# Kernel optimization log

Measured on AMD Instinct MI355X. Metric: run time of the kernel, lower is better.

## Reference

```python
import jax, jax.numpy as jnp
import numpy as np

EPS = 1e-6
LAMBDA_INIT = 0.8

def rmsnorm(x, g):
    return x * jax.lax.rsqrt(jnp.mean(x * x, axis=-1, keepdims=True) + EPS) * g

def diff_attention(q_in, kv_in, Wq, Wk, Wv, Wo, lq1, lk1, lq2, lk2, causal):
    # q_in: [B,T,D], kv_in: [B,S,D]; Wq/Wk: [D, H*2*hs], Wv: [D, H*hs], Wo: [H*hs, D]
    B, T, _ = q_in.shape
    S = kv_in.shape[1]
    H, hs = lq1.shape
    q = (q_in @ Wq).reshape(B, T, H, 2, hs)
    k = (kv_in @ Wk).reshape(B, S, H, 2, hs)
    v = (kv_in @ Wv).reshape(B, S, H, hs)
    q1, q2 = q[..., 0, :], q[..., 1, :]
    k1, k2 = k[..., 0, :], k[..., 1, :]
    scale = 1.0 / np.sqrt(hs).astype(np.float32)
    a1 = jnp.einsum('bthd,bshd->bhts', q1, k1) * scale  # [B,H,T,S]
    a2 = jnp.einsum('bthd,bshd->bhts', q2, k2) * scale
    if causal:
        mask = jnp.tril(jnp.ones((T, S), dtype=bool))
        neg = jnp.asarray(-1e9, a1.dtype)
        a1 = jnp.where(mask, a1, neg)
        a2 = jnp.where(mask, a2, neg)
    s1 = jax.nn.softmax(a1, axis=-1)
    s2 = jax.nn.softmax(a2, axis=-1)
    lam = jnp.exp(jnp.sum(lq1 * lk1, -1)) - jnp.exp(jnp.sum(lq2 * lk2, -1)) + LAMBDA_INIT  # [H]
    attn = s1 - lam[None, :, None, None] * s2
    o = jnp.einsum('bhts,bshd->bthd', attn, v)  # [B,T,H,hs]
    # per-head RMSNorm (no affine) scaled by (1 - lambda_init), per Diff Transformer
    o = o * jax.lax.rsqrt(jnp.mean(o * o, -1, keepdims=True) + EPS) * (1.0 - LAMBDA_INIT)
    return o.reshape(B, T, H * hs) @ Wo

def swiglu(x, W1, W2, W3):
    return (jax.nn.silu(x @ W1) * (x @ W2)) @ W3

def setup_inputs():
    B, T, D, H, hs = 4, 1024, 1024, 16, 64
    Dff = 4 * D
    ks = jax.random.split(jax.random.key(0), 24)
    w = lambda i, shape, s=0.02: (jax.random.normal(ks[i], shape, jnp.float32) * s)
    return {
        'x': jax.random.normal(ks[0], (B, T, D), jnp.float32),
        'encoder_output': jax.random.normal(ks[1], (B, T, D), jnp.float32),
        'Wq_s': w(2, (D, H * 2 * hs)), 'Wk_s': w(3, (D, H * 2 * hs)),
        'Wv_s': w(4, (D, H * hs)), 'Wo_s': w(5, (H * hs, D)),
        'lq1_s': w(6, (H, hs), 0.1), 'lk1_s': w(7, (H, hs), 0.1),
        'lq2_s': w(8, (H, hs), 0.1), 'lk2_s': w(9, (H, hs), 0.1),
        'Wq_c': w(10, (D, H * 2 * hs)), 'Wk_c': w(11, (D, H * 2 * hs)),
        'Wv_c': w(12, (D, H * hs)), 'Wo_c': w(13, (H * hs, D)),
        'lq1_c': w(14, (H, hs), 0.1), 'lk1_c': w(15, (H, hs), 0.1),
        'lq2_c': w(16, (H, hs), 0.1), 'lk2_c': w(17, (H, hs), 0.1),
        'g_rms': jnp.ones((D,), jnp.float32),
        'W1': w(18, (D, Dff)), 'W2': w(19, (D, Dff)), 'W3': w(20, (Dff, D)),
    }

def reference(x, encoder_output, Wq_s, Wk_s, Wv_s, Wo_s, lq1_s, lk1_s, lq2_s, lk2_s,
              Wq_c, Wk_c, Wv_c, Wo_c, lq1_c, lk1_c, lq2_c, lk2_c,
              g_rms, W1, W2, W3):
    # dropout prob 0.0 -> identity (eval/reference mode)
    h = rmsnorm(x, g_rms)
    h = diff_attention(h, h, Wq_s, Wk_s, Wv_s, Wo_s, lq1_s, lk1_s, lq2_s, lk2_s, causal=True) + h
    h = diff_attention(h, encoder_output, Wq_c, Wk_c, Wv_c, Wo_c, lq1_c, lk1_c, lq2_c, lk2_c, causal=False)
    h = h + h  # faithful to source: out = dropout(out) + out after cross-attention
    h = swiglu(rmsnorm(h, g_rms), W1, W2, W3) + h
    return h
```

## Files before the change

### kernel.cpp

```cpp
#include <hip/hip_runtime.h>

typedef __attribute__((ext_vector_type(8))) short s16x8;
typedef __attribute__((ext_vector_type(4))) float f32x4;
typedef unsigned short u16;

__device__ __forceinline__ float bu2f(u16 u) {
    union { unsigned int i; float f; } x; x.i = ((unsigned int)u) << 16; return x.f;
}
__device__ __forceinline__ u16 f2bu(float f) {
    union { float f; unsigned int i; } x; x.f = f;
    unsigned int r = x.i + 0x7fffu + ((x.i >> 16) & 1u);
    return (u16)(r >> 16);
}

__device__ __forceinline__ void gld_lds16(const void* g, void* l) {
    __builtin_amdgcn_global_load_lds(
        (const __attribute__((address_space(1))) unsigned int*)g,
        (__attribute__((address_space(3))) unsigned int*)l, 16, 0, 0);
}
#define WAIT_VM0()   asm volatile("s_waitcnt vmcnt(0)" ::: "memory")
#define WAIT_LGKM0() asm volatile("s_waitcnt lgkmcnt(0)" ::: "memory")
#define MEMBAR()     asm volatile("" ::: "memory")

__global__ __launch_bounds__(256)
void transpose_k(const float* __restrict__ src, u16* __restrict__ dst, int R, int C) {
    __shared__ u16 t[32][33];
    int bx = blockIdx.x * 32, by = blockIdx.y * 32;
    int x = bx + threadIdx.x;
#pragma unroll
    for (int k = 0; k < 4; ++k)
        t[threadIdx.y + k * 8][threadIdx.x] = f2bu(src[(size_t)(by + threadIdx.y + k * 8) * C + x]);
    __syncthreads();
    int x2 = by + threadIdx.x;
#pragma unroll
    for (int k = 0; k < 4; ++k)
        dst[(size_t)(bx + threadIdx.y + k * 8) * R + x2] = t[threadIdx.x][threadIdx.y + k * 8];
}

__global__ __launch_bounds__(256)
void convert_k(const float* __restrict__ a, u16* __restrict__ o, int n4) {
    int i = blockIdx.x * 256 + threadIdx.x;
    if (i >= n4) return;
    float4 v = ((const float4*)a)[i];
    ushort4 u;
    u.x = f2bu(v.x); u.y = f2bu(v.y); u.z = f2bu(v.z); u.w = f2bu(v.w);
    ((ushort4*)o)[i] = u;
}

__global__ __launch_bounds__(256)
void rmsnorm_k(const float* __restrict__ x, const float* __restrict__ g, u16* __restrict__ y) {
    const int row = blockIdx.x, tid = threadIdx.x;
    float4 v = ((const float4*)(x + (size_t)row * 1024))[tid];
    float ss = v.x * v.x + v.y * v.y + v.z * v.z + v.w * v.w;
#pragma unroll
    for (int off = 32; off; off >>= 1) ss += __shfl_xor(ss, off, 64);
    __shared__ float red[4];
    if ((tid & 63) == 0) red[tid >> 6] = ss;
    __syncthreads();
    float tot = red[0] + red[1] + red[2] + red[3];
    float sc = rsqrtf(tot * (1.f / 1024.f) + 1e-6f);
    float4 gv = ((const float4*)g)[tid];
    ushort4 o;
    o.x = f2bu(v.x * sc * gv.x);
    o.y = f2bu(v.y * sc * gv.y);
    o.z = f2bu(v.z * sc * gv.z);
    o.w = f2bu(v.w * sc * gv.w);
    ((ushort4*)(y + (size_t)row * 1024))[tid] = o;
}

__global__ __launch_bounds__(256)
void silumul_k(const u16* __restrict__ a, const u16* __restrict__ b, u16* __restrict__ o, int n4) {
    int i = blockIdx.x * 256 + threadIdx.x;
    if (i >= n4) return;
    ushort4 ua = ((const ushort4*)a)[i], ub = ((const ushort4*)b)[i];
    ushort4 uo;
    {
        float v = bu2f(ua.x); uo.x = f2bu(v / (1.f + __expf(-v)) * bu2f(ub.x));
        v = bu2f(ua.y); uo.y = f2bu(v / (1.f + __expf(-v)) * bu2f(ub.y));
        v = bu2f(ua.z); uo.z = f2bu(v / (1.f + __expf(-v)) * bu2f(ub.z));
        v = bu2f(ua.w); uo.w = f2bu(v / (1.f + __expf(-v)) * bu2f(ub.w));
    }
    ((ushort4*)o)[i] = uo;
}

template <int TM>
__global__ __launch_bounds__(256, 2)
void gemm_bt(const u16* __restrict__ A, const u16* __restrict__ Bt, void* __restrict__ C,
             const void* __restrict__ res, int M, int N, int K, int mode) {
    constexpr int MI = TM / 32;
    __shared__ u16 sA[TM * 32];
    __shared__ u16 sB[128 * 32];
    const int tid = threadIdx.x;
    const int w = tid >> 6, lane = tid & 63, q4 = lane >> 4, l16 = lane & 15;
    const int m0 = blockIdx.y * TM, n0 = blockIdx.x * 128;
    const int wm = (w >> 1) * (TM / 2), wn = (w & 1) * 64;

    const f32x4 fzero = {0.f, 0.f, 0.f, 0.f};
    f32x4 acc[MI][4];
#pragma unroll
    for (int i = 0; i < MI; ++i)
#pragma unroll
        for (int j = 0; j < 4; ++j) acc[i][j] = fzero;

    const int r0 = tid >> 2, c0 = (tid & 3) * 8;

    for (int k0 = 0; k0 < K; k0 += 32) {
        gld_lds16(A + (size_t)(m0 + r0) * K + k0 + c0, &sA[tid * 8]);
        if (TM == 128)
            gld_lds16(A + (size_t)(m0 + 64 + r0) * K + k0 + c0, &sA[(256 + tid) * 8]);
        gld_lds16(Bt + (size_t)(n0 + r0) * K + k0 + c0, &sB[tid * 8]);
        gld_lds16(Bt + (size_t)(n0 + 64 + r0) * K + k0 + c0, &sB[(256 + tid) * 8]);
        WAIT_VM0();
        __syncthreads();
        s16x8 af[MI], bfr[4];
#pragma unroll
        for (int i = 0; i < MI; ++i) af[i] = *(const s16x8*)&sA[(wm + i * 16 + l16) * 32 + q4 * 8];
#pragma unroll
        for (int j = 0; j < 4; ++j) bfr[j] = *(const s16x8*)&sB[(wn + j * 16 + l16) * 32 + q4 * 8];
#pragma unroll
        for (int i = 0; i < MI; ++i)
#pragma unroll
            for (int j = 0; j < 4; ++j)
                acc[i][j] = __builtin_amdgcn_mfma_f32_16x16x32_bf16(af[i], bfr[j], acc[i][j], 0, 0, 0);
        __syncthreads();
    }

    const size_t QBSZ = (size_t)4096 * 2048;
    const size_t FSZ  = (size_t)4096 * 4096;
#pragma unroll
    for (int i = 0; i < MI; ++i)
#pragma unroll
        for (int j = 0; j < 4; ++j)
#pragma unroll
            for (int r = 0; r < 4; ++r) {
                int m = m0 + wm + i * 16 + q4 * 4 + r;
                int n = n0 + wn + j * 16 + l16;
                float v = acc[i][j][r];
                if (mode == 0) {
                    ((u16*)C)[(size_t)m * N + n] = f2bu(v);
                } else if (mode == 1) {
                    ((u16*)C)[(size_t)m * N + n] = f2bu(v + bu2f(((const u16*)res)[(size_t)m * N + n]));
                } else if (mode == 2) {
                    ((float*)C)[(size_t)m * N + n] = 2.f * v;
                } else if (mode == 4) {
                    ((float*)C)[(size_t)m * N + n] = v + ((const float*)res)[(size_t)m * N + n];
                } else if (mode == 5) {
                    if (n < 2048) ((u16*)C)[(size_t)m * 2048 + n] = f2bu(v);
                    else if (n < 4096) ((u16*)C)[QBSZ + (size_t)m * 2048 + (n - 2048)] = f2bu(v);
                    else {
                        int nn = n - 4096, hh = nn >> 6, d = nn & 63, b = m >> 10, s = m & 1023;
                        ((u16*)C)[2 * QBSZ + ((size_t)((b * 16 + hh) * 64 + d)) * 1024 + s] = f2bu(v);
                    }
                } else if (mode == 6) {
                    if (n < 2048) ((u16*)C)[(size_t)m * 2048 + n] = f2bu(v);
                    else {
                        int nn = n - 2048, hh = nn >> 6, d = nn & 63, b = m >> 10, s = m & 1023;
                        ((u16*)C)[QBSZ + ((size_t)((b * 16 + hh) * 64 + d)) * 1024 + s] = f2bu(v);
                    }
                } else {
                    if (n < 4096) ((u16*)C)[(size_t)m * 4096 + n] = f2bu(v);
                    else ((u16*)C)[FSZ + (size_t)m * 4096 + (n - 4096)] = f2bu(v);
                }
            }
}

template <bool CAUSAL>
__global__ __launch_bounds__(256, 2)
void diff_flash(const u16* __restrict__ Q, const u16* __restrict__ Kg, const u16* __restrict__ Vt,
                u16* __restrict__ O, const float* __restrict__ lq1, const float* __restrict__ lk1,
                const float* __restrict__ lq2, const float* __restrict__ lk2, int T, int S) {
    __shared__ u16 sK1[2][64 * 64];
    __shared__ u16 sK2[2][64 * 64];
    __shared__ u16 sV[2][64 * 64];
    __shared__ u16 sP[4][16 * 72];

    const int tid = threadIdx.x;
    const int w = tid >> 6, lane = tid & 63, q4 = lane >> 4, l16 = lane & 15;
    const int h = blockIdx.x, b = blockIdx.y, zt = blockIdx.z, t0 = zt * 64;
    const f32x4 fzero = {0.f, 0.f, 0.f, 0.f};

    float d1 = 0.f, d2 = 0.f;
    for (int d = 0; d < 64; ++d) {
        d1 += lq1[h * 64 + d] * lk1[h * 64 + d];
        d2 += lq2[h * 64 + d] * lk2[h * 64 + d];
    }
    const float lam = __expf(d1) - __expf(d2) + 0.8f;

    s16x8 qf[2][2];
    {
        const size_t qrow = (size_t)(b * T + t0 + w * 16 + l16) * 2048 + h * 128;
#pragma unroll
        for (int c = 0; c < 2; ++c)
#pragma unroll
            for (int kk = 0; kk < 2; ++kk)
                qf[c][kk] = *(const s16x8*)&Q[qrow + c * 64 + kk * 32 + q4 * 8];
    }

    f32x4 o1[4], o2[4];
    float ms1[4], ls1[4], ms2[4], ls2[4];
#pragma unroll
    for (int jn = 0; jn < 4; ++jn) { o1[jn] = fzero; o2[jn] = fzero; }
#pragma unroll
    for (int r = 0; r < 4; ++r) { ms1[r] = ms2[r] = -1e30f; ls1[r] = ls2[r] = 0.f; }

    const int ntiles = CAUSAL ? (zt + 1) : (S / 64);
    const int rk = tid >> 3, ck = (tid & 7) * 8;

    auto stage = [&](int buf, int s0) {
        const size_t kb = (size_t)(b * S + s0 + rk) * 2048 + h * 128 + ck;
        gld_lds16(&Kg[kb], &sK1[buf][tid * 8]);
        gld_lds16(&Kg[kb + (size_t)32 * 2048], &sK1[buf][(256 + tid) * 8]);
        gld_lds16(&Kg[kb + 64], &sK2[buf][tid * 8]);
        gld_lds16(&Kg[kb + (size_t)32 * 2048 + 64], &sK2[buf][(256 + tid) * 8]);
        const size_t vb = (size_t)((b * 16 + h) * 64 + rk) * 1024 + s0 + ck;
        gld_lds16(&Vt[vb], &sV[buf][tid * 8]);
        gld_lds16(&Vt[vb + (size_t)32 * 1024], &sV[buf][(256 + tid) * 8]);
    };

    stage(0, 0);
    for (int it = 0; it < ntiles; ++it) {
        WAIT_VM0();
        __syncthreads();
        if (it + 1 < ntiles) stage((it + 1) & 1, (it + 1) * 64);
        const int buf = it & 1, s0 = it * 64;
        const bool diag = CAUSAL && (it == ntiles - 1);

        auto comp_step = [&](const u16* sK, const u16* sVb, const s16x8* qfc,
                             float* m, float* l, f32x4* o) {
            f32x4 sc[4];
#pragma unroll
            for (int j = 0; j < 4; ++j) sc[j] = fzero;
#pragma unroll
            for (int j = 0; j < 4; ++j)
#pragma unroll
                for (int kk = 0; kk < 2; ++kk) {
                    s16x8 kf = *(const s16x8*)&sK[(j * 16 + l16) * 64 + kk * 32 + q4 * 8];
                    sc[j] = __builtin_amdgcn_mfma_f32_16x16x32_bf16(qfc[kk], kf, sc[j], 0, 0, 0);
                }
            float p[4][4];
#pragma unroll
            for (int j = 0; j < 4; ++j)
#pragma unroll
                for (int r = 0; r < 4; ++r) {
                    float v = sc[j][r] * 0.125f;
                    if (diag && (s0 + j * 16 + l16 > t0 + w * 16 + q4 * 4 + r)) v = -1e9f;
                    p[j][r] = v;
                }
            float mx[4];
#pragma unroll
            for (int r = 0; r < 4; ++r)
                mx[r] = fmaxf(fmaxf(p[0][r], p[1][r]), fmaxf(p[2][r], p[3][r]));
#pragma unroll
            for (int off = 8; off; off >>= 1)
#pragma unroll
                for (int r = 0; r < 4; ++r) mx[r] = fmaxf(mx[r], __shfl_xor(mx[r], off, 16));
            float alpha[4];
#pragma unroll
            for (int r = 0; r < 4; ++r) {
                float mn = fmaxf(m[r], mx[r]);
                alpha[r] = __expf(m[r] - mn);
                m[r] = mn;
            }
            float rs[4];
#pragma unroll
            for (int r = 0; r < 4; ++r) {
                float s0r = 0.f;
#pragma unroll
                for (int j = 0; j < 4; ++j) { p[j][r] = __expf(p[j][r] - m[r]); s0r += p[j][r]; }
                rs[r] = s0r;
            }
#pragma unroll
            for (int off = 8; off; off >>= 1)
#pragma unroll
                for (int r = 0; r < 4; ++r) rs[r] += __shfl_xor(rs[r], off, 16);
#pragma unroll
            for (int r = 0; r < 4; ++r) l[r] = l[r] * alpha[r] + rs[r];
#pragma unroll
            for (int jn = 0; jn < 4; ++jn)
#pragma unroll
                for (int r = 0; r < 4; ++r) o[jn][r] *= alpha[r];
#pragma unroll
            for (int j = 0; j < 4; ++j)
#pragma unroll
                for (int r = 0; r < 4; ++r)
                    sP[w][(q4 * 4 + r) * 72 + j * 16 + l16] = f2bu(p[j][r]);
            WAIT_LGKM0();
            s16x8 pa0 = *(const s16x8*)&sP[w][l16 * 72 + q4 * 8];
            s16x8 pa1 = *(const s16x8*)&sP[w][l16 * 72 + 32 + q4 * 8];
#pragma unroll
            for (int jn = 0; jn < 4; ++jn) {
                s16x8 vf0 = *(const s16x8*)&sVb[(jn * 16 + l16) * 64 + q4 * 8];
                o[jn] = __builtin_amdgcn_mfma_f32_16x16x32_bf16(pa0, vf0, o[jn], 0, 0, 0);
                s16x8 vf1 = *(const s16x8*)&sVb[(jn * 16 + l16) * 64 + 32 + q4 * 8];
                o[jn] = __builtin_amdgcn_mfma_f32_16x16x32_bf16(pa1, vf1, o[jn], 0, 0, 0);
            }
            MEMBAR();
        };
        comp_step(sK1[buf], sV[buf], qf[0], ms1, ls1, o1);
        comp_step(sK2[buf], sV[buf], qf[1], ms2, ls2, o2);
    }

    float inv1[4], inv2[4];
#pragma unroll
    for (int r = 0; r < 4; ++r) { inv1[r] = 1.f / ls1[r]; inv2[r] = lam / ls2[r]; }
    float val[4][4];
    float ss[4] = {0.f, 0.f, 0.f, 0.f};
#pragma unroll
    for (int jn = 0; jn < 4; ++jn)
#pragma unroll
        for (int r = 0; r < 4; ++r) {
            float v = o1[jn][r] * inv1[r] - o2[jn][r] * inv2[r];
            val[jn][r] = v;
            ss[r] += v * v;
        }
#pragma unroll
    for (int off = 8; off; off >>= 1)
#pragma unroll
        for (int r = 0; r < 4; ++r) ss[r] += __shfl_xor(ss[r], off, 16);
#pragma unroll
    for (int r = 0; r < 4; ++r) ss[r] = rsqrtf(ss[r] * (1.f / 64.f) + 1e-6f) * 0.2f;
#pragma unroll
    for (int jn = 0; jn < 4; ++jn)
#pragma unroll
        for (int r = 0; r < 4; ++r)
            O[(size_t)(b * T + t0 + w * 16 + q4 * 4 + r) * 1024 + h * 64 + jn * 16 + l16] =
                f2bu(val[jn][r] * ss[r]);
}

extern "C" void kernel_launch(void* const* d_in, const int* in_sizes, int n_in,
                              void* d_out, int out_size, void* d_ws, size_t ws_size,
                              hipStream_t stream) {
    (void)in_sizes; (void)n_in; (void)out_size; (void)ws_size;
    const float* x     = (const float*)d_in[0];
    const float* enc   = (const float*)d_in[1];
    const float* Wq_s  = (const float*)d_in[2];
    const float* Wk_s  = (const float*)d_in[3];
    const float* Wv_s  = (const float*)d_in[4];
    const float* Wo_s  = (const float*)d_in[5];
    const float* lq1_s = (const float*)d_in[6];
    const float* lk1_s = (const float*)d_in[7];
    const float* lq2_s = (const float*)d_in[8];
    const float* lk2_s = (const float*)d_in[9];
    const float* Wq_c  = (const float*)d_in[10];
    const float* Wk_c  = (const float*)d_in[11];
    const float* Wv_c  = (const float*)d_in[12];
    const float* Wo_c  = (const float*)d_in[13];
    const float* lq1_c = (const float*)d_in[14];
    const float* lk1_c = (const float*)d_in[15];
    const float* lq2_c = (const float*)d_in[16];
    const float* lk2_c = (const float*)d_in[17];
    const float* g_rms = (const float*)d_in[18];
    const float* W1    = (const float*)d_in[19];
    const float* W2    = (const float*)d_in[20];
    const float* W3    = (const float*)d_in[21];

    char* ws = (char*)d_ws;
    size_t off = 0;
    auto ab = [&](size_t elems) -> u16* { u16* p = (u16*)(ws + off); off += elems * 2; return p; };
    u16* WqkvTs = ab((size_t)5120 * 1024);
    u16* WoTs   = ab((size_t)1024 * 1024);
    u16* WqTc   = ab((size_t)2048 * 1024);
    u16* WkvTc  = ab((size_t)3072 * 1024);
    u16* WoTc   = ab((size_t)1024 * 1024);
    u16* W12T   = ab((size_t)8192 * 1024);
    u16* W3T    = ab((size_t)1024 * 4096);
    char* pool = ws + off;
    u16* h0   = ab((size_t)4096 * 1024);
    u16* encb = ab((size_t)4096 * 1024);
    u16* Qb   = ab((size_t)4096 * 2048);
    u16* Kb   = ab((size_t)4096 * 2048);
    u16* Vt   = ab((size_t)4096 * 1024);
    u16* Ob   = ab((size_t)4096 * 1024);
    u16* fa   = (u16*)pool;
    u16* fb   = (u16*)(pool + (size_t)4096 * 4096 * 2);
    u16* h1   = ab((size_t)4096 * 1024);
    float* h2 = (float*)(ws + off); off += (size_t)4096 * 1024 * 4;
    u16* rn   = ab((size_t)4096 * 1024);

    dim3 tb(32, 8);
    transpose_k<<<dim3(64, 32), tb, 0, stream>>>(Wq_s, WqkvTs, 1024, 2048);
    transpose_k<<<dim3(64, 32), tb, 0, stream>>>(Wk_s, WqkvTs + (size_t)2048 * 1024, 1024, 2048);
    transpose_k<<<dim3(32, 32), tb, 0, stream>>>(Wv_s, WqkvTs + (size_t)4096 * 1024, 1024, 1024);
    transpose_k<<<dim3(32, 32), tb, 0, stream>>>(Wo_s, WoTs, 1024, 1024);
    transpose_k<<<dim3(64, 32), tb, 0, stream>>>(Wq_c, WqTc, 1024, 2048);
    transpose_k<<<dim3(64, 32), tb, 0, stream>>>(Wk_c, WkvTc, 1024, 2048);
    transpose_k<<<dim3(32, 32), tb, 0, stream>>>(Wv_c, WkvTc + (size_t)2048 * 1024, 1024, 1024);
    transpose_k<<<dim3(32, 32), tb, 0, stream>>>(Wo_c, WoTc, 1024, 1024);
    transpose_k<<<dim3(128, 32), tb, 0, stream>>>(W1, W12T, 1024, 4096);
    transpose_k<<<dim3(128, 32), tb, 0, stream>>>(W2, W12T + (size_t)4096 * 1024, 1024, 4096);
    transpose_k<<<dim3(32, 128), tb, 0, stream>>>(W3, W3T, 4096, 1024);

    rmsnorm_k<<<4096, 256, 0, stream>>>(x, g_rms, h0);
    convert_k<<<4096, 256, 0, stream>>>(enc, encb, 4096 * 1024 / 4);

    gemm_bt<128><<<dim3(40, 32), 256, 0, stream>>>(h0, WqkvTs, Qb, nullptr, 4096, 5120, 1024, 5);
    diff_flash<true><<<dim3(16, 4, 16), 256, 0, stream>>>(Qb, Kb, Vt, Ob, lq1_s, lk1_s, lq2_s, lk2_s, 1024, 1024);
    gemm_bt<64><<<dim3(8, 64), 256, 0, stream>>>(Ob, WoTs, h1, h0, 4096, 1024, 1024, 1);

    gemm_bt<128><<<dim3(16, 32), 256, 0, stream>>>(h1, WqTc, Qb, nullptr, 4096, 2048, 1024, 0);
    gemm_bt<128><<<dim3(24, 32), 256, 0, stream>>>(encb, WkvTc, Kb, nullptr, 4096, 3072, 1024, 6);
    diff_flash<false><<<dim3(16, 4, 16), 256, 0, stream>>>(Qb, Kb, Vt, Ob, lq1_c, lk1_c, lq2_c, lk2_c, 1024, 1024);
    gemm_bt<64><<<dim3(8, 64), 256, 0, stream>>>(Ob, WoTc, h2, nullptr, 4096, 1024, 1024, 2);

    rmsnorm_k<<<4096, 256, 0, stream>>>(h2, g_rms, rn);
    gemm_bt<128><<<dim3(64, 32), 256, 0, stream>>>(rn, W12T, fa, nullptr, 4096, 8192, 1024, 7);
    silumul_k<<<16384, 256, 0, stream>>>(fa, fb, fa, 4096 * 4096 / 4);
    gemm_bt<64><<<dim3(8, 64), 256, 0, stream>>>(fa, W3T, (float*)d_out, h2, 4096, 1024, 4096, 4);
}
```

Baseline: 870.5 us.

## Transpose attention MFMA layout, swizzle LDS, reverse causal tile order, batch transposes

```diff
diff --git a/kernel.cpp b/kernel.cpp
--- a/kernel.cpp
+++ b/kernel.cpp
@@ -23,7 +23,10 @@
 #define MEMBAR()     asm volatile("" ::: "memory")
 
 __global__ __launch_bounds__(256)
-void transpose_k(const float* __restrict__ src, u16* __restrict__ dst, int R, int C) {
+void transpose4_k(const float* s0, const float* s1, const float* s2, const float* s3,
+                  u16* d0, u16* d1, u16* d2, u16* d3, int R, int C) {
+    const float* src = blockIdx.z == 0 ? s0 : blockIdx.z == 1 ? s1 : blockIdx.z == 2 ? s2 : s3;
+    u16* dst = blockIdx.z == 0 ? d0 : blockIdx.z == 1 ? d1 : blockIdx.z == 2 ? d2 : d3;
     __shared__ u16 t[32][33];
     int bx = blockIdx.x * 32, by = blockIdx.y * 32;
     int x = bx + threadIdx.x;
@@ -172,11 +175,13 @@
     __shared__ u16 sK1[2][64 * 64];
     __shared__ u16 sK2[2][64 * 64];
     __shared__ u16 sV[2][64 * 64];
-    __shared__ u16 sP[4][16 * 72];
+    __shared__ u16 sP[4][16 * 64];
 
     const int tid = threadIdx.x;
     const int w = tid >> 6, lane = tid & 63, q4 = lane >> 4, l16 = lane & 15;
-    const int h = blockIdx.x, b = blockIdx.y, zt = blockIdx.z, t0 = zt * 64;
+    const int h = blockIdx.x, b = blockIdx.y;
+    const int zt = CAUSAL ? (gridDim.z - 1 - blockIdx.z) : blockIdx.z;
+    const int t0 = zt * 64;
     const f32x4 fzero = {0.f, 0.f, 0.f, 0.f};
 
     float d1 = 0.f, d2 = 0.f;
@@ -197,25 +202,28 @@
     }
 
     f32x4 o1[4], o2[4];
-    float ms1[4], ls1[4], ms2[4], ls2[4];
+    float ms1 = -1e30f, ls1 = 0.f, ms2 = -1e30f, ls2 = 0.f;
 #pragma unroll
     for (int jn = 0; jn < 4; ++jn) { o1[jn] = fzero; o2[jn] = fzero; }
-#pragma unroll
-    for (int r = 0; r < 4; ++r) { ms1[r] = ms2[r] = -1e30f; ls1[r] = ls2[r] = 0.f; }
 
     const int ntiles = CAUSAL ? (zt + 1) : (S / 64);
-    const int rk = tid >> 3, ck = (tid & 7) * 8;
+    const int rk = tid >> 3;
+    const int ckk = (((tid & 7) - rk) & 7) * 8;
 
     auto stage = [&](int buf, int s0) {
-        const size_t kb = (size_t)(b * S + s0 + rk) * 2048 + h * 128 + ck;
-        gld_lds16(&Kg[kb], &sK1[buf][tid * 8]);
-        gld_lds16(&Kg[kb + (size_t)32 * 2048], &sK1[buf][(256 + tid) * 8]);
-        gld_lds16(&Kg[kb + 64], &sK2[buf][tid * 8]);
-        gld_lds16(&Kg[kb + (size_t)32 * 2048 + 64], &sK2[buf][(256 + tid) * 8]);
-        const size_t vb = (size_t)((b * 16 + h) * 64 + rk) * 1024 + s0 + ck;
-        gld_lds16(&Vt[vb], &sV[buf][tid * 8]);
-        gld_lds16(&Vt[vb + (size_t)32 * 1024], &sV[buf][(256 + tid) * 8]);
+        const size_t kb = (size_t)(b * S + s0 + rk) * 2048 + h * 128;
+        gld_lds16(&Kg[kb + ckk], &sK1[buf][tid * 8]);
+        gld_lds16(&Kg[kb + (size_t)32 * 2048 + ckk], &sK1[buf][(256 + tid) * 8]);
+        gld_lds16(&Kg[kb + 64 + ckk], &sK2[buf][tid * 8]);
+        gld_lds16(&Kg[kb + (size_t)32 * 2048 + 64 + ckk], &sK2[buf][(256 + tid) * 8]);
+        const size_t vb = (size_t)((b * 16 + h) * 64 + rk) * 1024 + s0;
+        gld_lds16(&Vt[vb + ckk], &sV[buf][tid * 8]);
+        gld_lds16(&Vt[vb + (size_t)32 * 1024 + ckk], &sV[buf][(256 + tid) * 8]);
     };
+
+    u16* const sPw = sP[w];
+    const int slot0 = ((0 * 4 + q4 + l16) & 7) * 8;
+    const int slot1 = ((1 * 4 + q4 + l16) & 7) * 8;
 
     stage(0, 0);
     for (int it = 0; it < ntiles; ++it) {
@@ -225,106 +233,98 @@
         const int buf = it & 1, s0 = it * 64;
         const bool diag = CAUSAL && (it == ntiles - 1);
 
-        auto comp_step = [&](const u16* sK, const u16* sVb, const s16x8* qfc,
-                             float* m, float* l, f32x4* o) {
+        s16x8 vf[4][2];
+#pragma unroll
+        for (int jn = 0; jn < 4; ++jn) {
+            vf[jn][0] = *(const s16x8*)&sV[buf][(jn * 16 + l16) * 64 + slot0];
+            vf[jn][1] = *(const s16x8*)&sV[buf][(jn * 16 + l16) * 64 + slot1];
+        }
+
+        auto comp_step = [&](const u16* sK, const s16x8* qkk, float& m, float& l, f32x4* o) {
             f32x4 sc[4];
 #pragma unroll
-            for (int j = 0; j < 4; ++j) sc[j] = fzero;
-#pragma unroll
-            for (int j = 0; j < 4; ++j)
-#pragma unroll
-                for (int kk = 0; kk < 2; ++kk) {
-                    s16x8 kf = *(const s16x8*)&sK[(j * 16 + l16) * 64 + kk * 32 + q4 * 8];
-                    sc[j] = __builtin_amdgcn_mfma_f32_16x16x32_bf16(qfc[kk], kf, sc[j], 0, 0, 0);
+            for (int js = 0; js < 4; ++js) sc[js] = fzero;
+#pragma unroll
+            for (int js = 0; js < 4; ++js) {
+                s16x8 kf0 = *(const s16x8*)&sK[(js * 16 + l16) * 64 + slot0];
+                sc[js] = __builtin_amdgcn_mfma_f32_16x16x32_bf16(kf0, qkk[0], sc[js], 0, 0, 0);
+                s16x8 kf1 = *(const s16x8*)&sK[(js * 16 + l16) * 64 + slot1];
+                sc[js] = __builtin_amdgcn_mfma_f32_16x16x32_bf16(kf1, qkk[1], sc[js], 0, 0, 0);
+            }
+            float p[4][4];
+#pragma unroll
+            for (int js = 0; js < 4; ++js)
+#pragma unroll
+                for (int r = 0; r < 4; ++r) {
+                    float v = sc[js][r] * 0.125f;
+                    if (diag && (s0 + js * 16 + q4 * 4 + r > t0 + w * 16 + l16)) v = -1e9f;
+                    p[js][r] = v;
                 }
-            float p[4][4];
-#pragma unroll
-            for (int j = 0; j < 4; ++j)
-#pragma unroll
-                for (int r = 0; r < 4; ++r) {
-                    float v = sc[j][r] * 0.125f;
-                    if (diag && (s0 + j * 16 + l16 > t0 + w * 16 + q4 * 4 + r)) v = -1e9f;
-                    p[j][r] = v;
-                }
-            float mx[4];
-#pragma unroll
-            for (int r = 0; r < 4; ++r)
-                mx[r] = fmaxf(fmaxf(p[0][r], p[1][r]), fmaxf(p[2][r], p[3][r]));
-#pragma unroll
-            for (int off = 8; off; off >>= 1)
-#pragma unroll
-                for (int r = 0; r < 4; ++r) mx[r] = fmaxf(mx[r], __shfl_xor(mx[r], off, 16));
-            float alpha[4];
-#pragma unroll
-            for (int r = 0; r < 4; ++r) {
-                float mn = fmaxf(m[r], mx[r]);
-                alpha[r] = __expf(m[r] - mn);
-                m[r] = mn;
+            float mx = p[0][0];
+#pragma unroll
+            for (int js = 0; js < 4; ++js)
+#pragma unroll
+                for (int r = 0; r < 4; ++r) mx = fmaxf(mx, p[js][r]);
+            mx = fmaxf(mx, __shfl_xor(mx, 16, 64));
+            mx = fmaxf(mx, __shfl_xor(mx, 32, 64));
+            float mn = fmaxf(m, mx);
+            float alpha = __expf(m - mn);
+            m = mn;
+            float rs = 0.f;
+#pragma unroll
+            for (int js = 0; js < 4; ++js)
+#pragma unroll
+                for (int r = 0; r < 4; ++r) { p[js][r] = __expf(p[js][r] - mn); rs += p[js][r]; }
+            rs += __shfl_xor(rs, 16, 64);
+            rs += __shfl_xor(rs, 32, 64);
+            l = l * alpha + rs;
+#pragma unroll
+            for (int jn = 0; jn < 4; ++jn) o[jn] *= alpha;
+#pragma unroll
+            for (int js = 0; js < 4; ++js) {
+                ushort4 pk;
+                pk.x = f2bu(p[js][0]); pk.y = f2bu(p[js][1]);
+                pk.z = f2bu(p[js][2]); pk.w = f2bu(p[js][3]);
+                int sl = ((js * 2 + (q4 >> 1) + l16) & 7) * 8 + (q4 & 1) * 4;
+                *(ushort4*)&sPw[l16 * 64 + sl] = pk;
             }
-            float rs[4];
-#pragma unroll
-            for (int r = 0; r < 4; ++r) {
-                float s0r = 0.f;
-#pragma unroll
-                for (int j = 0; j < 4; ++j) { p[j][r] = __expf(p[j][r] - m[r]); s0r += p[j][r]; }
-                rs[r] = s0r;
-            }
-#pragma unroll
-            for (int off = 8; off; off >>= 1)
-#pragma unroll
-                for (int r = 0; r < 4; ++r) rs[r] += __shfl_xor(rs[r], off, 16);
-#pragma unroll
-            for (int r = 0; r < 4; ++r) l[r] = l[r] * alpha[r] + rs[r];
-#pragma unroll
-            for (int jn = 0; jn < 4; ++jn)
-#pragma unroll
-                for (int r = 0; r < 4; ++r) o[jn][r] *= alpha[r];
-#pragma unroll
-            for (int j = 0; j < 4; ++j)
-#pragma unroll
-                for (int r = 0; r < 4; ++r)
-                    sP[w][(q4 * 4 + r) * 72 + j * 16 + l16] = f2bu(p[j][r]);
             WAIT_LGKM0();
-            s16x8 pa0 = *(const s16x8*)&sP[w][l16 * 72 + q4 * 8];
-            s16x8 pa1 = *(const s16x8*)&sP[w][l16 * 72 + 32 + q4 * 8];
+            s16x8 pb0 = *(const s16x8*)&sPw[l16 * 64 + slot0];
+            s16x8 pb1 = *(const s16x8*)&sPw[l16 * 64 + slot1];
 #pragma unroll
             for (int jn = 0; jn < 4; ++jn) {
-                s16x8 vf0 = *(const s16x8*)&sVb[(jn * 16 + l16) * 64 + q4 * 8];
-                o[jn] = __builtin_amdgcn_mfma_f32_16x16x32_bf16(pa0, vf0, o[jn], 0, 0, 0);
-                s16x8 vf1 = *(const s16x8*)&sVb[(jn * 16 + l16) * 64 + 32 + q4 * 8];
-                o[jn] = __builtin_amdgcn_mfma_f32_16x16x32_bf16(pa1, vf1, o[jn], 0, 0, 0);
+                o[jn] = __builtin_amdgcn_mfma_f32_16x16x32_bf16(vf[jn][0], pb0, o[jn], 0, 0, 0);
+                o[jn] = __builtin_amdgcn_mfma_f32_16x16x32_bf16(vf[jn][1], pb1, o[jn], 0, 0, 0);
             }
             MEMBAR();
         };
-        comp_step(sK1[buf], sV[buf], qf[0], ms1, ls1, o1);
-        comp_step(sK2[buf], sV[buf], qf[1], ms2, ls2, o2);
-    }
-
-    float inv1[4], inv2[4];
-#pragma unroll
-    for (int r = 0; r < 4; ++r) { inv1[r] = 1.f / ls1[r]; inv2[r] = lam / ls2[r]; }
+        comp_step(sK1[buf], qf[0], ms1, ls1, o1);
+        comp_step(sK2[buf], qf[1], ms2, ls2, o2);
+        __syncthreads();
+    }
+
+    const float inv1 = 1.f / ls1, inv2 = lam / ls2;
     float val[4][4];
-    float ss[4] = {0.f, 0.f, 0.f, 0.f};
+    float ss = 0.f;
 #pragma unroll
     for (int jn = 0; jn < 4; ++jn)
 #pragma unroll
         for (int r = 0; r < 4; ++r) {
-            float v = o1[jn][r] * inv1[r] - o2[jn][r] * inv2[r];
+            float v = o1[jn][r] * inv1 - o2[jn][r] * inv2;
             val[jn][r] = v;
-            ss[r] += v * v;
+            ss += v * v;
         }
-#pragma unroll
-    for (int off = 8; off; off >>= 1)
-#pragma unroll
-        for (int r = 0; r < 4; ++r) ss[r] += __shfl_xor(ss[r], off, 16);
-#pragma unroll
-    for (int r = 0; r < 4; ++r) ss[r] = rsqrtf(ss[r] * (1.f / 64.f) + 1e-6f) * 0.2f;
-#pragma unroll
-    for (int jn = 0; jn < 4; ++jn)
-#pragma unroll
-        for (int r = 0; r < 4; ++r)
-            O[(size_t)(b * T + t0 + w * 16 + q4 * 4 + r) * 1024 + h * 64 + jn * 16 + l16] =
-                f2bu(val[jn][r] * ss[r]);
+    ss += __shfl_xor(ss, 16, 64);
+    ss += __shfl_xor(ss, 32, 64);
+    const float scl = rsqrtf(ss * (1.f / 64.f) + 1e-6f) * 0.2f;
+    const size_t orow = (size_t)(b * T + t0 + w * 16 + l16) * 1024 + h * 64;
+#pragma unroll
+    for (int jn = 0; jn < 4; ++jn) {
+        ushort4 ov;
+        ov.x = f2bu(val[jn][0] * scl); ov.y = f2bu(val[jn][1] * scl);
+        ov.z = f2bu(val[jn][2] * scl); ov.w = f2bu(val[jn][3] * scl);
+        *(ushort4*)&O[orow + jn * 16 + q4 * 4] = ov;
+    }
 }
 
 extern "C" void kernel_launch(void* const* d_in, const int* in_sizes, int n_in,
@@ -378,17 +378,15 @@
     u16* rn   = ab((size_t)4096 * 1024);
 
     dim3 tb(32, 8);
-    transpose_k<<<dim3(64, 32), tb, 0, stream>>>(Wq_s, WqkvTs, 1024, 2048);
-    transpose_k<<<dim3(64, 32), tb, 0, stream>>>(Wk_s, WqkvTs + (size_t)2048 * 1024, 1024, 2048);
-    transpose_k<<<dim3(32, 32), tb, 0, stream>>>(Wv_s, WqkvTs + (size_t)4096 * 1024, 1024, 1024);
-    transpose_k<<<dim3(32, 32), tb, 0, stream>>>(Wo_s, WoTs, 1024, 1024);
-    transpose_k<<<dim3(64, 32), tb, 0, stream>>>(Wq_c, WqTc, 1024, 2048);
-    transpose_k<<<dim3(64, 32), tb, 0, stream>>>(Wk_c, WkvTc, 1024, 2048);
-    transpose_k<<<dim3(32, 32), tb, 0, stream>>>(Wv_c, WkvTc + (size_t)2048 * 1024, 1024, 1024);
-    transpose_k<<<dim3(32, 32), tb, 0, stream>>>(Wo_c, WoTc, 1024, 1024);
-    transpose_k<<<dim3(128, 32), tb, 0, stream>>>(W1, W12T, 1024, 4096);
-    transpose_k<<<dim3(128, 32), tb, 0, stream>>>(W2, W12T + (size_t)4096 * 1024, 1024, 4096);
-    transpose_k<<<dim3(32, 128), tb, 0, stream>>>(W3, W3T, 4096, 1024);
+    transpose4_k<<<dim3(64, 32, 4), tb, 0, stream>>>(
+        Wq_s, Wk_s, Wq_c, Wk_c,
+        WqkvTs, WqkvTs + (size_t)2048 * 1024, WqTc, WkvTc, 1024, 2048);
+    transpose4_k<<<dim3(32, 32, 4), tb, 0, stream>>>(
+        Wv_s, Wo_s, Wv_c, Wo_c,
+        WqkvTs + (size_t)4096 * 1024, WoTs, WkvTc + (size_t)2048 * 1024, WoTc, 1024, 1024);
+    transpose4_k<<<dim3(128, 32, 2), tb, 0, stream>>>(
+        W1, W2, W1, W2, W12T, W12T + (size_t)4096 * 1024, W12T, W12T, 1024, 4096);
+    transpose4_k<<<dim3(32, 128, 1), tb, 0, stream>>>(W3, W3, W3, W3, W3T, W3T, W3T, W3T, 4096, 1024);
 
     rmsnorm_k<<<4096, 256, 0, stream>>>(x, g_rms, h0);
     convert_k<<<4096, 256, 0, stream>>>(enc, encb, 4096 * 1024 / 4);
```

Result: faster. 757.8 us (-12.9%).
